# Optimization experiments

Measured on AMD Instinct MI355X. Metric: run time of the kernel, lower is better.

The kernel has to match this reference:

```python
import jax, jax.numpy as jnp
import numpy as np

N = 20000
E = 320000
F_IN = 256
HID = 32
HEADS = 8
EDGE_DIM = HID // 4  # 8
NEG_SLOPE = 0.2


def _gat_conv(x, src, dst, e_emb, W, att_s, att_d, W_e, att_e, bias, H, C):
    """PyG-style GATConv with edge_dim, add_self_loops=True (fill_value='mean'), concat heads."""
    n = x.shape[0]
    loop = jnp.arange(n, dtype=src.dtype)
    # self-loop edge_attr = scatter-mean of edge_attr by dst (0 for isolated nodes)
    deg = jax.ops.segment_sum(jnp.ones_like(dst, dtype=x.dtype), dst, num_segments=n)
    e_mean = jax.ops.segment_sum(e_emb, dst, num_segments=n) / jnp.maximum(deg, 1.0)[:, None]
    src_a = jnp.concatenate([src, loop])
    dst_a = jnp.concatenate([dst, loop])
    e_all = jnp.concatenate([e_emb, e_mean], axis=0)  # [E+N, edge_dim]

    h = (x @ W).reshape(n, H, C)                      # [N,H,C]
    a_src = jnp.einsum('nhc,hc->nh', h, att_s)        # [N,H]
    a_dst = jnp.einsum('nhc,hc->nh', h, att_d)
    he = (e_all @ W_e).reshape(-1, H, C)              # [E+N,H,C]
    a_edge = jnp.einsum('ehc,hc->eh', he, att_e)      # [E+N,H]

    alpha = jax.nn.leaky_relu(a_src[src_a] + a_dst[dst_a] + a_edge, NEG_SLOPE)
    # segment softmax over destination nodes
    amax = jax.ops.segment_max(alpha, dst_a, num_segments=n)
    alpha = jnp.exp(alpha - amax[dst_a])
    denom = jax.ops.segment_sum(alpha, dst_a, num_segments=n)
    alpha = alpha / (denom[dst_a] + 1e-16)

    msg = h[src_a] * alpha[:, :, None]                # [E+N,H,C]
    out = jax.ops.segment_sum(msg, dst_a, num_segments=n)  # [N,H,C]
    return out.reshape(n, H * C) + bias


def setup_inputs() -> dict:
    key = jax.random.key(0)
    ks = jax.random.split(key, 16)

    def glorot(k, shape):
        fan_in, fan_out = shape[0], shape[-1]
        s = np.sqrt(6.0 / (fan_in + fan_out))
        return jax.random.uniform(k, shape, jnp.float32, -s, s)

    x = jax.random.normal(ks[0], (N, F_IN), jnp.float32)
    edge_index = jax.random.randint(ks[1], (2, E), 0, N, jnp.int32)
    edge_attr = jax.random.uniform(ks[2], (E, 2), jnp.float32)

    # spatial_embed: Linear(2 -> EDGE_DIM)
    Wse = glorot(ks[3], (2, EDGE_DIM))
    bse = jnp.zeros((EDGE_DIM,), jnp.float32)
    # conv1: in=F_IN, heads=HEADS, out=HID, edge_dim=EDGE_DIM
    W1 = glorot(ks[4], (F_IN, HEADS * HID))
    as1 = glorot(ks[5], (HEADS, HID))
    ad1 = glorot(ks[6], (HEADS, HID))
    We1 = glorot(ks[7], (EDGE_DIM, HEADS * HID))
    ae1 = glorot(ks[8], (HEADS, HID))
    b1 = jnp.zeros((HEADS * HID,), jnp.float32)
    # conv2: in=HEADS*HID, heads=1, out=HID
    W2 = glorot(ks[9], (HEADS * HID, HID))
    as2 = glorot(ks[10], (1, HID))
    ad2 = glorot(ks[11], (1, HID))
    We2 = glorot(ks[12], (EDGE_DIM, HID))
    ae2 = glorot(ks[13], (1, HID))
    b2 = jnp.zeros((HID,), jnp.float32)

    return {"x": x, "edge_index": edge_index, "edge_attr": edge_attr,
            "Wse": Wse, "bse": bse,
            "W1": W1, "as1": as1, "ad1": ad1, "We1": We1, "ae1": ae1, "b1": b1,
            "W2": W2, "as2": as2, "ad2": ad2, "We2": We2, "ae2": ae2, "b2": b2}


def reference(x, edge_index, edge_attr, Wse, bse,
              W1, as1, ad1, We1, ae1, b1,
              W2, as2, ad2, We2, ae2, b2):
    src, dst = edge_index[0], edge_index[1]
    e = jax.nn.relu(edge_attr @ Wse + bse)            # [E, EDGE_DIM]
    h = _gat_conv(x, src, dst, e, W1, as1, ad1, We1, ae1, b1, HEADS, HID)
    h = jax.nn.relu(h)                                # dropout inactive (eval)
    out = _gat_conv(h, src, dst, e, W2, as2, ad2, We2, ae2, b2, 1, HID)
    return out
```

## Files before the change

kernel.cpp:

```cpp
#include <hip/hip_runtime.h>
#include <float.h>


typedef short v8s __attribute__((ext_vector_type(8)));
typedef float v4f __attribute__((ext_vector_type(4)));

__device__ __forceinline__ ushort f2bf(float f) {
  unsigned u = __float_as_uint(f);
  u = (u + 0x7FFF + ((u >> 16) & 1)) >> 16;
  return (ushort)u;
}
__device__ __forceinline__ float bf2f(ushort h) {
  return __uint_as_float(((unsigned)h) << 16);
}

__global__ void k_deg(const int* __restrict__ dst, int* __restrict__ deg, int E) {
  int e = blockIdx.x * blockDim.x + threadIdx.x;
  if (e < E) atomicAdd(&deg[dst[e]], 1);
}

__global__ __launch_bounds__(1024) void k_scan(const int* __restrict__ deg,
                                               int* __restrict__ row_ptr, int N) {
  __shared__ int part[1024];
  int tid = threadIdx.x;
  int chunk = (N + 1023) / 1024;
  int lo = tid * chunk;
  if (lo > N) lo = N;
  int hi = lo + chunk;
  if (hi > N) hi = N;
  int s = 0;
  for (int i = lo; i < hi; i++) s += deg[i] + 1;
  part[tid] = s;
  __syncthreads();
  for (int off = 1; off < 1024; off <<= 1) {
    int v = 0;
    if (tid >= off) v = part[tid - off];
    __syncthreads();
    part[tid] += v;
    __syncthreads();
  }
  int base = part[tid] - s;
  for (int i = lo; i < hi; i++) { row_ptr[i] = base; base += deg[i] + 1; }
  if (tid == 1023) row_ptr[N] = part[1023];
}

__global__ void k_scatter(const int* __restrict__ src, const int* __restrict__ dst,
                          const int* __restrict__ row_ptr, int* __restrict__ cursor,
                          const float* __restrict__ aed1_lin, const float* __restrict__ aed2_lin,
                          int* __restrict__ csr_src, float* __restrict__ csr_aed1,
                          float* __restrict__ csr_aed2, int* __restrict__ selfpos,
                          int E, int N) {
  int i = blockIdx.x * blockDim.x + threadIdx.x;
  if (i >= E + N) return;
  if (i < E) {
    int d = dst[i];
    int pos = row_ptr[d] + atomicAdd(&cursor[d], 1);
    csr_src[pos] = src[i];
    const float4* a4 = (const float4*)(aed1_lin + (size_t)i * 8);
    *(float4*)(csr_aed1 + (size_t)pos * 8)     = a4[0];
    *(float4*)(csr_aed1 + (size_t)pos * 8 + 4) = a4[1];
    csr_aed2[pos] = aed2_lin[i];
  } else {
    int n = i - E;
    int pos = row_ptr[n] + atomicAdd(&cursor[n], 1);
    csr_src[pos] = n;
    selfpos[n] = pos;
  }
}

__global__ void k_prep(const float* __restrict__ We1, const float* __restrict__ ae1,
                       const float* __restrict__ We2, const float* __restrict__ ae2,
                       float* __restrict__ M1, float* __restrict__ m2) {
  int t = threadIdx.x;
  if (t < 64) {
    int k = t >> 3, h = t & 7;
    float s = 0.f;
    for (int c = 0; c < 32; c++) s += We1[k * 256 + h * 32 + c] * ae1[h * 32 + c];
    M1[k * 8 + h] = s;
  } else if (t < 72) {
    int k = t - 64;
    float s = 0.f;
    for (int c = 0; c < 32; c++) s += We2[k * 32 + c] * ae2[c];
    m2[k] = s;
  }
}

__global__ __launch_bounds__(256) void k_transpose(const float* __restrict__ W1,
                                                   ushort* __restrict__ Bt) {
  __shared__ float tile[32][33];
  int bx = blockIdx.x & 7, by = blockIdx.x >> 3;
  int tx = threadIdx.x & 31, ty = threadIdx.x >> 5;
  for (int r = ty; r < 32; r += 8)
    tile[r][tx] = W1[(size_t)(by * 32 + r) * 256 + bx * 32 + tx];
  __syncthreads();
  for (int r = ty; r < 32; r += 8)
    Bt[(size_t)(bx * 32 + r) * 256 + by * 32 + tx] = f2bf(tile[tx][r]);
}

__global__ void k_edge_fused(const float* __restrict__ ea, const float* __restrict__ Wse,
                             const float* __restrict__ bse, const float* __restrict__ M1,
                             const float* __restrict__ m2,
                             float* __restrict__ aed1, float* __restrict__ aed2, int E) {
  __shared__ float sW[16], sb[8], sM[64], sm2[8];
  int t = threadIdx.x;
  if (t < 16) sW[t] = Wse[t];
  if (t < 8) sb[t] = bse[t];
  if (t < 64) sM[t] = M1[t];
  if (t >= 64 && t < 72) sm2[t - 64] = m2[t - 64];
  __syncthreads();
  int e = blockIdx.x * blockDim.x + t;
  if (e >= E) return;
  float2 av = ((const float2*)ea)[e];
  float e8[8];
#pragma unroll
  for (int k = 0; k < 8; k++)
    e8[k] = fmaxf(av.x * sW[k] + av.y * sW[8 + k] + sb[k], 0.f);
  float o[8];
#pragma unroll
  for (int h = 0; h < 8; h++) {
    float s = 0.f;
#pragma unroll
    for (int k = 0; k < 8; k++) s += e8[k] * sM[k * 8 + h];
    o[h] = s;
  }
  *(float4*)(aed1 + (size_t)e * 8)     = make_float4(o[0], o[1], o[2], o[3]);
  *(float4*)(aed1 + (size_t)e * 8 + 4) = make_float4(o[4], o[5], o[6], o[7]);
  float s2 = 0.f;
#pragma unroll
  for (int k = 0; k < 8; k++) s2 += e8[k] * sm2[k];
  aed2[e] = s2;
}

__global__ void k_selfmean(const int* __restrict__ row_ptr, const int* __restrict__ selfpos,
                           float* __restrict__ csr_aed1, float* __restrict__ csr_aed2,
                           int N) {
  int i = blockIdx.x * blockDim.x + threadIdx.x;
  if (i >= N * 8) return;
  int n = i >> 3, h = i & 7;
  int begin = row_ptr[n], end = row_ptr[n + 1];
  int sp = selfpos[n];
  int deg = end - begin - 1;
  float inv = 1.f / (float)(deg > 1 ? deg : 1);
  float s = 0.f, s2 = 0.f;
  for (int p = begin; p < end; p++) {
    if (p == sp) continue;
    s += csr_aed1[(size_t)p * 8 + h];
    if (h == 0) s2 += csr_aed2[p];
  }
  csr_aed1[(size_t)sp * 8 + h] = s * inv;
  if (h == 0) csr_aed2[sp] = s2 * inv;
}

__global__ __launch_bounds__(256) void k_gemm1_mfma(const float* __restrict__ A,
                                                    const ushort* __restrict__ Bt,
                                                    ushort* __restrict__ h1b, int M) {
  __shared__ ushort sA[64 * 40];
  __shared__ ushort sB[256 * 40];
  int t = threadIdx.x;
  int wave = t >> 6, lane = t & 63;
  int m0 = blockIdx.x * 64;
  int c = lane & 15, kg = lane >> 4;
  v4f acc[4][4];
#pragma unroll
  for (int a = 0; a < 4; a++)
#pragma unroll
    for (int b = 0; b < 4; b++) acc[a][b] = (v4f)(0.f);
  int arow = t >> 2;
  int akoff = (t & 3) * 8;
  bool aval = (m0 + arow) < M;
  const float* aptr = A + (size_t)(m0 + arow) * 256 + akoff;
  const ushort* bptr = Bt + (size_t)t * 256;
  for (int k0 = 0; k0 < 256; k0 += 32) {
    float4 v0 = make_float4(0.f, 0.f, 0.f, 0.f), v1 = v0;
    if (aval) { v0 = *(const float4*)(aptr + k0); v1 = *(const float4*)(aptr + k0 + 4); }
    ushort* dst = &sA[arow * 40 + akoff];
    dst[0] = f2bf(v0.x); dst[1] = f2bf(v0.y); dst[2] = f2bf(v0.z); dst[3] = f2bf(v0.w);
    dst[4] = f2bf(v1.x); dst[5] = f2bf(v1.y); dst[6] = f2bf(v1.z); dst[7] = f2bf(v1.w);
    *(v8s*)&sB[t * 40 + 0]  = *(const v8s*)(bptr + k0 + 0);
    *(v8s*)&sB[t * 40 + 8]  = *(const v8s*)(bptr + k0 + 8);
    *(v8s*)&sB[t * 40 + 16] = *(const v8s*)(bptr + k0 + 16);
    *(v8s*)&sB[t * 40 + 24] = *(const v8s*)(bptr + k0 + 24);
    __syncthreads();
    v8s af[4], bfr[4];
#pragma unroll
    for (int mt = 0; mt < 4; mt++) af[mt] = *(v8s*)&sA[(mt * 16 + c) * 40 + kg * 8];
#pragma unroll
    for (int nt = 0; nt < 4; nt++) bfr[nt] = *(v8s*)&sB[(wave * 64 + nt * 16 + c) * 40 + kg * 8];
#pragma unroll
    for (int mt = 0; mt < 4; mt++)
#pragma unroll
      for (int nt = 0; nt < 4; nt++)
        acc[mt][nt] = __builtin_amdgcn_mfma_f32_16x16x32_bf16(af[mt], bfr[nt], acc[mt][nt], 0, 0, 0);
    __syncthreads();
  }
#pragma unroll
  for (int mt = 0; mt < 4; mt++) {
#pragma unroll
    for (int i = 0; i < 4; i++) {
      int m = m0 + mt * 16 + kg * 4 + i;
      if (m < M) {
#pragma unroll
        for (int nt = 0; nt < 4; nt++)
          h1b[(size_t)m * 256 + wave * 64 + nt * 16 + c] = f2bf(acc[mt][nt][i]);
      }
    }
  }
}

__global__ void k_attn1(const ushort* __restrict__ h1b, const float* __restrict__ as1,
                        const float* __restrict__ ad1, float* __restrict__ asv,
                        float* __restrict__ adv, int N) {
  int i = blockIdx.x * blockDim.x + threadIdx.x;
  if (i >= N * 8) return;
  int n = i >> 3, h = i & 7;
  const ushort* hp = h1b + (size_t)n * 256 + h * 32;
  const float* ap = as1 + h * 32;
  const float* dp = ad1 + h * 32;
  float s1 = 0.f, s2 = 0.f;
#pragma unroll
  for (int c = 0; c < 32; c++) {
    float v = bf2f(hp[c]);
    s1 += v * ap[c];
    s2 += v * dp[c];
  }
  asv[i] = s1;
  adv[i] = s2;
}

__global__ __launch_bounds__(64) void k_conv1(
    const int* __restrict__ row_ptr, const int* __restrict__ csr_src,
    const float* __restrict__ csr_aed1, const float* __restrict__ asv,
    const float* __restrict__ adv, const ushort* __restrict__ h1b,
    const float* __restrict__ b1, float* __restrict__ h2, int N) {
  int n = blockIdx.x;
  int lane = threadIdx.x;
  int h = lane >> 3;
  int sub = lane & 7;
  __shared__ float sw[64 * 8];
  __shared__ int ssrc[64];
  __shared__ float sm[8], sl[8], sadv[8];
  int begin = row_ptr[n], end = row_ptr[n + 1];
  if (lane < 8) { sm[lane] = -FLT_MAX; sl[lane] = 0.f; sadv[lane] = adv[(size_t)n * 8 + lane]; }
  float4 acc = make_float4(0.f, 0.f, 0.f, 0.f);
  for (int cs = begin; cs < end; cs += 64) {
    int c = min(64, end - cs);
    __syncthreads();
    if (lane < c) ssrc[lane] = csr_src[cs + lane];
    __syncthreads();
    for (int idx = lane; idx < c * 8; idx += 64) {
      int el = idx >> 3, hh = idx & 7;
      float a = asv[(size_t)ssrc[el] * 8 + hh] + sadv[hh] +
                csr_aed1[(size_t)(cs + el) * 8 + hh];
      a = a > 0.f ? a : 0.2f * a;
      sw[idx] = a;
    }
    __syncthreads();
    float mloc = -FLT_MAX;
    for (int el = sub; el < c; el += 8) mloc = fmaxf(mloc, sw[el * 8 + h]);
#pragma unroll
    for (int o = 1; o < 8; o <<= 1) mloc = fmaxf(mloc, __shfl_xor(mloc, o));
    float mold = sm[h];
    float mnew = fmaxf(mold, mloc);
    float scale = __expf(mold - mnew);
    float lloc = 0.f;
    for (int el = sub; el < c; el += 8) {
      float w = __expf(sw[el * 8 + h] - mnew);
      sw[el * 8 + h] = w;
      lloc += w;
    }
#pragma unroll
    for (int o = 1; o < 8; o <<= 1) lloc += __shfl_xor(lloc, o);
    __syncthreads();
    if (sub == 0) { sm[h] = mnew; sl[h] = sl[h] * scale + lloc; }
    acc.x *= scale; acc.y *= scale; acc.z *= scale; acc.w *= scale;
    for (int el = 0; el < c; el++) {
      float w = sw[el * 8 + h];
      ushort4 hv = *(const ushort4*)(h1b + (size_t)ssrc[el] * 256 + lane * 4);
      acc.x += w * bf2f(hv.x);
      acc.y += w * bf2f(hv.y);
      acc.z += w * bf2f(hv.z);
      acc.w += w * bf2f(hv.w);
    }
  }
  __syncthreads();
  float inv = 1.f / (sl[h] + 1e-16f);
  float4 bv = *(const float4*)(b1 + lane * 4);
  float4 o4;
  o4.x = fmaxf(acc.x * inv + bv.x, 0.f);
  o4.y = fmaxf(acc.y * inv + bv.y, 0.f);
  o4.z = fmaxf(acc.z * inv + bv.z, 0.f);
  o4.w = fmaxf(acc.w * inv + bv.w, 0.f);
  *(float4*)(h2 + (size_t)n * 256 + lane * 4) = o4;
}

__global__ __launch_bounds__(256) void k_gemm2(const float* __restrict__ h2,
                                               const float* __restrict__ W2,
                                               const float* __restrict__ as2,
                                               const float* __restrict__ ad2,
                                               float* __restrict__ g2,
                                               float* __restrict__ asv2,
                                               float* __restrict__ adv2, int N) {
  __shared__ float xs[8 * 256];
  __shared__ float sas[32], sad[32];
  int t = threadIdx.x;
  if (t < 32) { sas[t] = as2[t]; sad[t] = ad2[t]; }
  int n0 = blockIdx.x * 8;
  for (int idx = t; idx < 8 * 256; idx += 256) {
    int node = n0 + (idx >> 8);
    xs[idx] = (node < N) ? h2[(size_t)node * 256 + (idx & 255)] : 0.f;
  }
  __syncthreads();
  int j = t >> 5, cc = t & 31;
  int node = n0 + j;
  float acc = 0.f;
#pragma unroll 8
  for (int k = 0; k < 256; k++) acc += xs[j * 256 + k] * W2[k * 32 + cc];
  float s1 = acc * sas[cc], s2 = acc * sad[cc];
#pragma unroll
  for (int o = 1; o < 32; o <<= 1) {
    s1 += __shfl_xor(s1, o);
    s2 += __shfl_xor(s2, o);
  }
  if (node < N) {
    g2[(size_t)node * 32 + cc] = acc;
    if (cc == 0) { asv2[node] = s1; adv2[node] = s2; }
  }
}

__global__ __launch_bounds__(64) void k_conv2(
    const int* __restrict__ row_ptr, const int* __restrict__ csr_src,
    const float* __restrict__ csr_aed2, const float* __restrict__ asv2,
    const float* __restrict__ adv2, const float* __restrict__ g2,
    const float* __restrict__ b2, float* __restrict__ out, int N) {
  int n = blockIdx.x;
  int lane = threadIdx.x;
  int sub = lane >> 3, q = lane & 7;
  __shared__ float sw[64];
  __shared__ int ssrc[64];
  int begin = row_ptr[n], end = row_ptr[n + 1];
  float advn = adv2[n];
  float m = -FLT_MAX, l = 0.f;
  float4 acc = make_float4(0.f, 0.f, 0.f, 0.f);
  for (int cs = begin; cs < end; cs += 64) {
    int c = min(64, end - cs);
    __syncthreads();
    float a = -FLT_MAX;
    if (lane < c) {
      int s = csr_src[cs + lane];
      ssrc[lane] = s;
      a = asv2[s] + advn + csr_aed2[cs + lane];
      a = a > 0.f ? a : 0.2f * a;
    }
    float cm = a;
#pragma unroll
    for (int o = 1; o < 64; o <<= 1) cm = fmaxf(cm, __shfl_xor(cm, o));
    float nm = fmaxf(m, cm);
    float sc = __expf(m - nm);
    float w = (lane < c) ? __expf(a - nm) : 0.f;
    float cl = w;
#pragma unroll
    for (int o = 1; o < 64; o <<= 1) cl += __shfl_xor(cl, o);
    l = l * sc + cl;
    m = nm;
    sw[lane] = w;
    __syncthreads();
    acc.x *= sc; acc.y *= sc; acc.z *= sc; acc.w *= sc;
    for (int el = sub; el < c; el += 8) {
      float w2 = sw[el];
      const float4 gv = *(const float4*)(g2 + (size_t)ssrc[el] * 32 + q * 4);
      acc.x += w2 * gv.x; acc.y += w2 * gv.y; acc.z += w2 * gv.z; acc.w += w2 * gv.w;
    }
  }
#pragma unroll
  for (int o = 8; o < 64; o <<= 1) {
    acc.x += __shfl_xor(acc.x, o);
    acc.y += __shfl_xor(acc.y, o);
    acc.z += __shfl_xor(acc.z, o);
    acc.w += __shfl_xor(acc.w, o);
  }
  if (lane < 8) {
    float inv = 1.f / (l + 1e-16f);
    float4 bv = *(const float4*)(b2 + lane * 4);
    float4 o4;
    o4.x = acc.x * inv + bv.x;
    o4.y = acc.y * inv + bv.y;
    o4.z = acc.z * inv + bv.z;
    o4.w = acc.w * inv + bv.w;
    *(float4*)(out + (size_t)n * 32 + lane * 4) = o4;
  }
}

extern "C" void kernel_launch(void* const* d_in, const int* in_sizes, int n_in,
                              void* d_out, int out_size, void* d_ws, size_t ws_size,
                              hipStream_t stream) {
  (void)n_in; (void)out_size; (void)ws_size;
  const float* x   = (const float*)d_in[0];
  const int*   ei  = (const int*)d_in[1];
  const float* ea  = (const float*)d_in[2];
  const float* Wse = (const float*)d_in[3];
  const float* bse = (const float*)d_in[4];
  const float* W1  = (const float*)d_in[5];
  const float* as1 = (const float*)d_in[6];
  const float* ad1 = (const float*)d_in[7];
  const float* We1 = (const float*)d_in[8];
  const float* ae1 = (const float*)d_in[9];
  const float* b1  = (const float*)d_in[10];
  const float* W2  = (const float*)d_in[11];
  const float* as2 = (const float*)d_in[12];
  const float* ad2 = (const float*)d_in[13];
  const float* We2 = (const float*)d_in[14];
  const float* ae2 = (const float*)d_in[15];
  const float* b2  = (const float*)d_in[16];
  const int N = in_sizes[0] / 256;
  const int E = in_sizes[1] / 2;
  const int* src = ei;
  const int* dst = ei + E;

  char* base = (char*)d_ws;
  size_t off = 0;
  auto alloc = [&](size_t bytes) -> char* {
    off = (off + 255) & ~(size_t)255;
    char* p = base + off;
    off += bytes;
    return p;
  };
  int*   deg      = (int*)alloc((size_t)N * 4);
  int*   cursor   = (int*)alloc((size_t)N * 4);
  size_t zero_bytes = (size_t)((char*)(cursor + N) - (char*)deg);
  int* row_ptr    = (int*)alloc((size_t)(N + 1) * 4);
  int* selfpos    = (int*)alloc((size_t)N * 4);
  int* csr_src    = (int*)alloc((size_t)(E + N) * 4);
  float* aed1_lin = (float*)alloc((size_t)E * 8 * 4);
  float* aed2_lin = (float*)alloc((size_t)E * 4);
  float* csr_aed1 = (float*)alloc((size_t)(E + N) * 8 * 4);
  float* csr_aed2 = (float*)alloc((size_t)(E + N) * 4);
  ushort* W1T     = (ushort*)alloc((size_t)256 * 256 * 2);
  ushort* h1b     = (ushort*)alloc((size_t)N * 256 * 2);
  float* asv1     = (float*)alloc((size_t)N * 8 * 4);
  float* adv1     = (float*)alloc((size_t)N * 8 * 4);
  float* h2       = (float*)alloc((size_t)N * 256 * 4);
  float* g2       = (float*)alloc((size_t)N * 32 * 4);
  float* asv2     = (float*)alloc((size_t)N * 4);
  float* adv2     = (float*)alloc((size_t)N * 4);
  float* M1       = (float*)alloc(64 * 4);
  float* m2       = (float*)alloc(8 * 4);

  hipMemsetAsync(deg, 0, zero_bytes, stream);
  k_deg<<<(E + 255) / 256, 256, 0, stream>>>(dst, deg, E);
  k_scan<<<1, 1024, 0, stream>>>(deg, row_ptr, N);
  k_prep<<<1, 128, 0, stream>>>(We1, ae1, We2, ae2, M1, m2);
  k_edge_fused<<<(E + 255) / 256, 256, 0, stream>>>(ea, Wse, bse, M1, m2, aed1_lin, aed2_lin, E);
  k_scatter<<<(E + N + 255) / 256, 256, 0, stream>>>(src, dst, row_ptr, cursor,
                                                     aed1_lin, aed2_lin,
                                                     csr_src, csr_aed1, csr_aed2, selfpos, E, N);
  k_selfmean<<<(N * 8 + 255) / 256, 256, 0, stream>>>(row_ptr, selfpos, csr_aed1, csr_aed2, N);
  k_transpose<<<64, 256, 0, stream>>>(W1, W1T);
  k_gemm1_mfma<<<(N + 63) / 64, 256, 0, stream>>>(x, W1T, h1b, N);
  k_attn1<<<(N * 8 + 255) / 256, 256, 0, stream>>>(h1b, as1, ad1, asv1, adv1, N);
  k_conv1<<<N, 64, 0, stream>>>(row_ptr, csr_src, csr_aed1, asv1, adv1, h1b, b1, h2, N);
  k_gemm2<<<(N + 7) / 8, 256, 0, stream>>>(h2, W2, as2, ad2, g2, asv2, adv2, N);
  k_conv2<<<N, 64, 0, stream>>>(row_ptr, csr_src, csr_aed2, asv2, adv2, g2, b2, (float*)d_out, N);
}
```

Baseline: 276.8 us.

## Fuse degree count, prep/transpose, attention dots into neighbors; store h2 as bf16

Folds the degree atomic count into the edge embedding kernel and merges the weight-prep and W1 transpose into one launch. It also computes the per-head source/destination attention logits in the GEMM1 epilogue using shuffles, which removes the k_attn1 pass. The intermediate h2 is now stored in bf16, halving its write and read traffic. The cost is fewer launches and less memory traffic, in exchange for extra precision loss in h2 and extra register/shared use in the GEMM epilogue.

```diff
diff --git a/kernel.cpp b/kernel.cpp
--- a/kernel.cpp
+++ b/kernel.cpp
@@ -12,11 +12,6 @@
 }
 __device__ __forceinline__ float bf2f(ushort h) {
   return __uint_as_float(((unsigned)h) << 16);
-}
-
-__global__ void k_deg(const int* __restrict__ dst, int* __restrict__ deg, int E) {
-  int e = blockIdx.x * blockDim.x + threadIdx.x;
-  if (e < E) atomicAdd(&deg[dst[e]], 1);
 }
 
 __global__ __launch_bounds__(1024) void k_scan(const int* __restrict__ deg,
@@ -68,25 +63,29 @@
   }
 }
 
-__global__ void k_prep(const float* __restrict__ We1, const float* __restrict__ ae1,
-                       const float* __restrict__ We2, const float* __restrict__ ae2,
-                       float* __restrict__ M1, float* __restrict__ m2) {
-  int t = threadIdx.x;
-  if (t < 64) {
-    int k = t >> 3, h = t & 7;
-    float s = 0.f;
-    for (int c = 0; c < 32; c++) s += We1[k * 256 + h * 32 + c] * ae1[h * 32 + c];
-    M1[k * 8 + h] = s;
-  } else if (t < 72) {
-    int k = t - 64;
-    float s = 0.f;
-    for (int c = 0; c < 32; c++) s += We2[k * 32 + c] * ae2[c];
-    m2[k] = s;
-  }
-}
-
-__global__ __launch_bounds__(256) void k_transpose(const float* __restrict__ W1,
-                                                   ushort* __restrict__ Bt) {
+__global__ __launch_bounds__(256) void k_prep_trans(const float* __restrict__ W1,
+                                                    const float* __restrict__ We1,
+                                                    const float* __restrict__ ae1,
+                                                    const float* __restrict__ We2,
+                                                    const float* __restrict__ ae2,
+                                                    ushort* __restrict__ Bt,
+                                                    float* __restrict__ M1,
+                                                    float* __restrict__ m2) {
+  if (blockIdx.x == 64) {
+    int t = threadIdx.x;
+    if (t < 64) {
+      int k = t >> 3, h = t & 7;
+      float s = 0.f;
+      for (int c = 0; c < 32; c++) s += We1[k * 256 + h * 32 + c] * ae1[h * 32 + c];
+      M1[k * 8 + h] = s;
+    } else if (t < 72) {
+      int k = t - 64;
+      float s = 0.f;
+      for (int c = 0; c < 32; c++) s += We2[k * 32 + c] * ae2[c];
+      m2[k] = s;
+    }
+    return;
+  }
   __shared__ float tile[32][33];
   int bx = blockIdx.x & 7, by = blockIdx.x >> 3;
   int tx = threadIdx.x & 31, ty = threadIdx.x >> 5;
@@ -97,10 +96,11 @@
     Bt[(size_t)(bx * 32 + r) * 256 + by * 32 + tx] = f2bf(tile[tx][r]);
 }
 
-__global__ void k_edge_fused(const float* __restrict__ ea, const float* __restrict__ Wse,
-                             const float* __restrict__ bse, const float* __restrict__ M1,
-                             const float* __restrict__ m2,
-                             float* __restrict__ aed1, float* __restrict__ aed2, int E) {
+__global__ void k_edge_fused(const float* __restrict__ ea, const int* __restrict__ dst,
+                             const float* __restrict__ Wse, const float* __restrict__ bse,
+                             const float* __restrict__ M1, const float* __restrict__ m2,
+                             float* __restrict__ aed1, float* __restrict__ aed2,
+                             int* __restrict__ deg, int E) {
   __shared__ float sW[16], sb[8], sM[64], sm2[8];
   int t = threadIdx.x;
   if (t < 16) sW[t] = Wse[t];
@@ -110,6 +110,7 @@
   __syncthreads();
   int e = blockIdx.x * blockDim.x + t;
   if (e >= E) return;
+  atomicAdd(&deg[dst[e]], 1);
   float2 av = ((const float2*)ea)[e];
   float e8[8];
 #pragma unroll
@@ -153,13 +154,20 @@
 
 __global__ __launch_bounds__(256) void k_gemm1_mfma(const float* __restrict__ A,
                                                     const ushort* __restrict__ Bt,
-                                                    ushort* __restrict__ h1b, int M) {
+                                                    const float* __restrict__ as1,
+                                                    const float* __restrict__ ad1,
+                                                    ushort* __restrict__ h1b,
+                                                    float* __restrict__ asv,
+                                                    float* __restrict__ adv, int M) {
   __shared__ ushort sA[64 * 40];
   __shared__ ushort sB[256 * 40];
+  __shared__ float sas[256], sad[256];
   int t = threadIdx.x;
   int wave = t >> 6, lane = t & 63;
   int m0 = blockIdx.x * 64;
   int c = lane & 15, kg = lane >> 4;
+  sas[t] = as1[t];
+  sad[t] = ad1[t];
   v4f acc[4][4];
 #pragma unroll
   for (int a = 0; a < 4; a++)
@@ -193,6 +201,7 @@
         acc[mt][nt] = __builtin_amdgcn_mfma_f32_16x16x32_bf16(af[mt], bfr[nt], acc[mt][nt], 0, 0, 0);
     __syncthreads();
   }
+  int colbase = wave * 64;
 #pragma unroll
   for (int mt = 0; mt < 4; mt++) {
 #pragma unroll
@@ -201,37 +210,34 @@
       if (m < M) {
 #pragma unroll
         for (int nt = 0; nt < 4; nt++)
-          h1b[(size_t)m * 256 + wave * 64 + nt * 16 + c] = f2bf(acc[mt][nt][i]);
+          h1b[(size_t)m * 256 + colbase + nt * 16 + c] = f2bf(acc[mt][nt][i]);
       }
-    }
-  }
-}
-
-__global__ void k_attn1(const ushort* __restrict__ h1b, const float* __restrict__ as1,
-                        const float* __restrict__ ad1, float* __restrict__ asv,
-                        float* __restrict__ adv, int N) {
-  int i = blockIdx.x * blockDim.x + threadIdx.x;
-  if (i >= N * 8) return;
-  int n = i >> 3, h = i & 7;
-  const ushort* hp = h1b + (size_t)n * 256 + h * 32;
-  const float* ap = as1 + h * 32;
-  const float* dp = ad1 + h * 32;
-  float s1 = 0.f, s2 = 0.f;
-#pragma unroll
-  for (int c = 0; c < 32; c++) {
-    float v = bf2f(hp[c]);
-    s1 += v * ap[c];
-    s2 += v * dp[c];
-  }
-  asv[i] = s1;
-  adv[i] = s2;
+      float s1a = acc[mt][0][i] * sas[colbase + c]      + acc[mt][1][i] * sas[colbase + 16 + c];
+      float s2a = acc[mt][0][i] * sad[colbase + c]      + acc[mt][1][i] * sad[colbase + 16 + c];
+      float s1b = acc[mt][2][i] * sas[colbase + 32 + c] + acc[mt][3][i] * sas[colbase + 48 + c];
+      float s2b = acc[mt][2][i] * sad[colbase + 32 + c] + acc[mt][3][i] * sad[colbase + 48 + c];
+#pragma unroll
+      for (int o = 1; o < 16; o <<= 1) {
+        s1a += __shfl_xor(s1a, o);
+        s2a += __shfl_xor(s2a, o);
+        s1b += __shfl_xor(s1b, o);
+        s2b += __shfl_xor(s2b, o);
+      }
+      if (c == 0 && m < M) {
+        asv[(size_t)m * 8 + 2 * wave]     = s1a;
+        adv[(size_t)m * 8 + 2 * wave]     = s2a;
+        asv[(size_t)m * 8 + 2 * wave + 1] = s1b;
+        adv[(size_t)m * 8 + 2 * wave + 1] = s2b;
+      }
+    }
+  }
 }
 
 __global__ __launch_bounds__(64) void k_conv1(
     const int* __restrict__ row_ptr, const int* __restrict__ csr_src,
     const float* __restrict__ csr_aed1, const float* __restrict__ asv,
     const float* __restrict__ adv, const ushort* __restrict__ h1b,
-    const float* __restrict__ b1, float* __restrict__ h2, int N) {
+    const float* __restrict__ b1, ushort* __restrict__ h2b, int N) {
   int n = blockIdx.x;
   int lane = threadIdx.x;
   int h = lane >> 3;
@@ -285,15 +291,15 @@
   __syncthreads();
   float inv = 1.f / (sl[h] + 1e-16f);
   float4 bv = *(const float4*)(b1 + lane * 4);
-  float4 o4;
-  o4.x = fmaxf(acc.x * inv + bv.x, 0.f);
-  o4.y = fmaxf(acc.y * inv + bv.y, 0.f);
-  o4.z = fmaxf(acc.z * inv + bv.z, 0.f);
-  o4.w = fmaxf(acc.w * inv + bv.w, 0.f);
-  *(float4*)(h2 + (size_t)n * 256 + lane * 4) = o4;
-}
-
-__global__ __launch_bounds__(256) void k_gemm2(const float* __restrict__ h2,
+  ushort4 o4;
+  o4.x = f2bf(fmaxf(acc.x * inv + bv.x, 0.f));
+  o4.y = f2bf(fmaxf(acc.y * inv + bv.y, 0.f));
+  o4.z = f2bf(fmaxf(acc.z * inv + bv.z, 0.f));
+  o4.w = f2bf(fmaxf(acc.w * inv + bv.w, 0.f));
+  *(ushort4*)(h2b + (size_t)n * 256 + lane * 4) = o4;
+}
+
+__global__ __launch_bounds__(256) void k_gemm2(const ushort* __restrict__ h2b,
                                                const float* __restrict__ W2,
                                                const float* __restrict__ as2,
                                                const float* __restrict__ ad2,
@@ -307,7 +313,7 @@
   int n0 = blockIdx.x * 8;
   for (int idx = t; idx < 8 * 256; idx += 256) {
     int node = n0 + (idx >> 8);
-    xs[idx] = (node < N) ? h2[(size_t)node * 256 + (idx & 255)] : 0.f;
+    xs[idx] = (node < N) ? bf2f(h2b[(size_t)node * 256 + (idx & 255)]) : 0.f;
   }
   __syncthreads();
   int j = t >> 5, cc = t & 31;
@@ -438,7 +444,7 @@
   ushort* h1b     = (ushort*)alloc((size_t)N * 256 * 2);
   float* asv1     = (float*)alloc((size_t)N * 8 * 4);
   float* adv1     = (float*)alloc((size_t)N * 8 * 4);
-  float* h2       = (float*)alloc((size_t)N * 256 * 4);
+  ushort* h2b     = (ushort*)alloc((size_t)N * 256 * 2);
   float* g2       = (float*)alloc((size_t)N * 32 * 4);
   float* asv2     = (float*)alloc((size_t)N * 4);
   float* adv2     = (float*)alloc((size_t)N * 4);
@@ -446,18 +452,16 @@
   float* m2       = (float*)alloc(8 * 4);
 
   hipMemsetAsync(deg, 0, zero_bytes, stream);
-  k_deg<<<(E + 255) / 256, 256, 0, stream>>>(dst, deg, E);
+  k_prep_trans<<<65, 256, 0, stream>>>(W1, We1, ae1, We2, ae2, W1T, M1, m2);
+  k_edge_fused<<<(E + 255) / 256, 256, 0, stream>>>(ea, dst, Wse, bse, M1, m2,
+                                                    aed1_lin, aed2_lin, deg, E);
   k_scan<<<1, 1024, 0, stream>>>(deg, row_ptr, N);
-  k_prep<<<1, 128, 0, stream>>>(We1, ae1, We2, ae2, M1, m2);
-  k_edge_fused<<<(E + 255) / 256, 256, 0, stream>>>(ea, Wse, bse, M1, m2, aed1_lin, aed2_lin, E);
   k_scatter<<<(E + N + 255) / 256, 256, 0, stream>>>(src, dst, row_ptr, cursor,
                                                      aed1_lin, aed2_lin,
                                                      csr_src, csr_aed1, csr_aed2, selfpos, E, N);
   k_selfmean<<<(N * 8 + 255) / 256, 256, 0, stream>>>(row_ptr, selfpos, csr_aed1, csr_aed2, N);
-  k_transpose<<<64, 256, 0, stream>>>(W1, W1T);
-  k_gemm1_mfma<<<(N + 63) / 64, 256, 0, stream>>>(x, W1T, h1b, N);
-  k_attn1<<<(N * 8 + 255) / 256, 256, 0, stream>>>(h1b, as1, ad1, asv1, adv1, N);
-  k_conv1<<<N, 64, 0, stream>>>(row_ptr, csr_src, csr_aed1, asv1, adv1, h1b, b1, h2, N);
-  k_gemm2<<<(N + 7) / 8, 256, 0, stream>>>(h2, W2, as2, ad2, g2, asv2, adv2, N);
+  k_gemm1_mfma<<<(N + 63) / 64, 256, 0, stream>>>(x, W1T, as1, ad1, h1b, asv1, adv1, N);
+  k_conv1<<<N, 64, 0, stream>>>(row_ptr, csr_src, csr_aed1, asv1, adv1, h1b, b1, h2b, N);
+  k_gemm2<<<(N + 7) / 8, 256, 0, stream>>>(h2b, W2, as2, ad2, g2, asv2, adv2, N);
   k_conv2<<<N, 64, 0, stream>>>(row_ptr, csr_src, csr_aed2, asv2, adv2, g2, b2, (float*)d_out, N);
 }
```

New measurement: 266.9 us. 1.04x faster.
